# Optimization experiments

Hardware: AMD Instinct MI355X
Metric: run time of the kernel (lower is better)

The kernel has to match this reference:

```python
import jax, jax.numpy as jnp
import numpy as np

B, C, IMG, P = 8, 6, 384, 16
DIM, HEADS, DEPTH, MLP, NCLS = 768, 12, 4, 3072, 1000
N = (IMG // P) ** 2            # 576 patches
DH = DIM // HEADS              # 64
PATCH_DIM = C * P * P          # 1536


def setup_inputs() -> dict:
    key = jax.random.key(0)
    ks = jax.random.split(key, 13)
    f = lambda k, shp, s=0.02: jax.random.normal(k, shp, jnp.float32) * s
    return {
        "x": jax.random.normal(ks[0], (B, C, IMG, IMG), jnp.float32),
        "patch_w": f(ks[1], (PATCH_DIM, DIM)),
        "patch_b": f(ks[2], (DIM,)),
        "ln1_g": jnp.ones((DEPTH, DIM), jnp.float32),
        "ln1_b": jnp.zeros((DEPTH, DIM), jnp.float32),
        "w_qkv": f(ks[3], (DEPTH, DIM, 3 * DIM)),
        "bias_att": f(ks[4], (DEPTH, HEADS, N, N), 0.5),
        "w_out": f(ks[5], (DEPTH, DIM, DIM)),
        "ln2_g": jnp.ones((DEPTH, DIM), jnp.float32),
        "ln2_b": jnp.zeros((DEPTH, DIM), jnp.float32),
        "w1": f(ks[6], (DEPTH, DIM, MLP)),
        "b1": f(ks[7], (DEPTH, MLP)),
        "w2": f(ks[8], (DEPTH, MLP, DIM)),
        "b2": f(ks[9], (DEPTH, DIM)),
        "lnh_g": jnp.ones((DIM,), jnp.float32),
        "lnh_b": jnp.zeros((DIM,), jnp.float32),
        "w_head": f(ks[10], (DIM, NCLS)),
        "b_head": f(ks[11], (NCLS,)),
    }


def _ln(x, g, b, eps=1e-5):
    m = x.mean(-1, keepdims=True)
    v = ((x - m) ** 2).mean(-1, keepdims=True)
    return (x - m) * jax.lax.rsqrt(v + eps) * g + b


def _patchify(x, patch_w, patch_b):
    # Rearrange 'b c (h p1) (w p2) -> b (h w) (p1 p2 c)' then Linear(patch_dim, dim)
    b = x.shape[0]
    g = IMG // P
    x = x.reshape(b, C, g, P, g, P).transpose(0, 2, 4, 3, 5, 1).reshape(b, g * g, PATCH_DIM)
    return x @ patch_w + patch_b


def _forward(x, patch_w, patch_b, ln1_g, ln1_b, w_qkv, bias_att, w_out,
             ln2_g, ln2_b, w1, b1, w2, b2, lnh_g, lnh_b, w_head, b_head):
    scale = DH ** -0.5
    tok = _patchify(x, patch_w, patch_b)  # [B, N, DIM]; pos_info='mul_att_normed' -> no pos_embed added

    def block(t, p):
        l1g, l1b, wqkv, bias, wout, l2g, l2b, ww1, bb1, ww2, bb2 = p
        h = _ln(t, l1g, l1b)
        qkv = h @ wqkv                                     # [B, N, 3*DIM]
        q, k, v = jnp.split(qkv, 3, axis=-1)
        rs = lambda a: a.reshape(t.shape[0], N, HEADS, DH).transpose(0, 2, 1, 3)
        q, k, v = rs(q), rs(k), rs(v)                      # [B, H, N, DH]
        dots = jnp.einsum('bhid,bhjd->bhij', q, k) * scale
        # mul_att_normed: softmax(qk) * softmax(bias), renormalized over keys
        attn = jax.nn.softmax(dots, axis=-1) * jax.nn.softmax(bias, axis=-1)[None]
        attn = attn / attn.sum(-1, keepdims=True)
        o = jnp.einsum('bhij,bhjd->bhid', attn, v)
        o = o.transpose(0, 2, 1, 3).reshape(t.shape[0], N, DIM) @ wout
        t = t + o
        h2 = _ln(t, l2g, l2b)
        t = t + (jax.nn.gelu(h2 @ ww1 + bb1, approximate=False) @ ww2 + bb2)
        return t, None

    tok, _ = jax.lax.scan(block, tok,
                          (ln1_g, ln1_b, w_qkv, bias_att, w_out,
                           ln2_g, ln2_b, w1, b1, w2, b2))
    pooled = tok.mean(axis=1)                              # mean-pool tokens
    return _ln(pooled, lnh_g, lnh_b) @ w_head + b_head     # [B, NCLS]


def reference(x, patch_w, patch_b, ln1_g, ln1_b, w_qkv, bias_att, w_out,
              ln2_g, ln2_b, w1, b1, w2, b2, lnh_g, lnh_b, w_head, b_head):
    return _forward(x, patch_w, patch_b, ln1_g, ln1_b, w_qkv, bias_att, w_out,
                    ln2_g, ln2_b, w1, b1, w2, b2, lnh_g, lnh_b, w_head, b_head)
```

## Files before the change

kernel.cpp:

```cpp
#include <hip/hip_runtime.h>
#include <hip/hip_bf16.h>

typedef __attribute__((ext_vector_type(8))) short bf16x8;
typedef __attribute__((ext_vector_type(4))) float f32x4;

#define DEVI __device__ __forceinline__

DEVI unsigned short f2bf_bits(float f) {
    __hip_bfloat16 h = __float2bfloat16(f);
    return *reinterpret_cast<unsigned short*>(&h);
}
DEVI float bfbits2f(unsigned short u) {
    __hip_bfloat16 h = *reinterpret_cast<__hip_bfloat16*>(&u);
    return __bfloat162float(h);
}

DEVI void gload_lds16(const void* g, void* lds) {
    __builtin_amdgcn_global_load_lds(
        (const __attribute__((address_space(1))) unsigned int*)g,
        (__attribute__((address_space(3))) unsigned int*)lds, 16, 0, 0);
}

template <int N> DEVI void wait_vm() {
    if constexpr (N == 0) asm volatile("s_waitcnt vmcnt(0)" ::: "memory");
    else if constexpr (N == 3) asm volatile("s_waitcnt vmcnt(3)" ::: "memory");
    else if constexpr (N == 6) asm volatile("s_waitcnt vmcnt(6)" ::: "memory");
    else if constexpr (N == 12) asm volatile("s_waitcnt vmcnt(12)" ::: "memory");
    __builtin_amdgcn_sched_barrier(0);
}

DEVI int2 remap_cm(int bid, int total, int nrow) {
    int q = total >> 3, r = total & 7, x = bid & 7, l = bid >> 3;
    int seq = (x < r ? x * (q + 1) : r * (q + 1) + (x - r) * q) + l;
    return {seq % nrow, seq / nrow};
}

__global__ __launch_bounds__(256) void patchify_kernel(const float* __restrict__ x,
                                                       unsigned short* __restrict__ patches)
{
    size_t t8 = (size_t)blockIdx.x * 256 + threadIdx.x;
    int jq = (int)(t8 % 48);
    size_t t = t8 / 48;
    int r = (int)(t % 384); t /= 384;
    int c = (int)(t % 6);
    int b = (int)(t / 6);
    int j = jq * 8;
    int gh = r >> 4, p1 = r & 15, gw = j >> 4, p2 = j & 15;
    int prow = b * 576 + gh * 24 + gw;
    int pcol = c * 256 + p1 * 16 + p2;
    const float* src = x + ((((size_t)b * 6 + c) * 384 + r) * 384 + j);
    float4 v0 = ((const float4*)src)[0];
    float4 v1 = ((const float4*)src)[1];
    ushort u[8] = { f2bf_bits(v0.x), f2bf_bits(v0.y), f2bf_bits(v0.z), f2bf_bits(v0.w),
                    f2bf_bits(v1.x), f2bf_bits(v1.y), f2bf_bits(v1.z), f2bf_bits(v1.w) };
    *(int4*)&patches[(size_t)prow * 1536 + pcol] = *(int4*)u;
}

__global__ __launch_bounds__(256) void convT_patch_kernel(const float* __restrict__ W,
                                                          __hip_bfloat16* __restrict__ Wt)
{
    __shared__ float tile[32][33];
    int n0 = blockIdx.x * 32, kp0 = blockIdx.y * 32;
    int tx = threadIdx.x & 31, ty = threadIdx.x >> 5;
#pragma unroll
    for (int i = 0; i < 4; i++) {
        int kp = kp0 + ty + 8 * i;
        int k = (kp & 255) * 6 + (kp >> 8);
        tile[ty + 8 * i][tx] = W[(size_t)k * 768 + n0 + tx];
    }
    __syncthreads();
#pragma unroll
    for (int i = 0; i < 4; i++)
        Wt[(size_t)(n0 + ty + 8 * i) * 1536 + kp0 + tx] = __float2bfloat16(tile[tx][ty + 8 * i]);
}

DEVI void convT_body(const float* __restrict__ W, __hip_bfloat16* __restrict__ Wt,
                     int K, int N, int k0, int n0, int tid)
{
    __shared__ float tile[32][33];
    int tx = tid & 31, ty = tid >> 5;
#pragma unroll
    for (int i = 0; i < 4; i++)
        tile[ty + 8 * i][tx] = W[(size_t)(k0 + ty + 8 * i) * N + n0 + tx];
    __syncthreads();
#pragma unroll
    for (int i = 0; i < 4; i++)
        Wt[(size_t)(n0 + ty + 8 * i) * K + k0 + tx] = __float2bfloat16(tile[tx][ty + 8 * i]);
}

__global__ __launch_bounds__(256) void convT4_kernel(const float* __restrict__ wqkv,
                                                     const float* __restrict__ wout,
                                                     const float* __restrict__ w1,
                                                     const float* __restrict__ w2,
                                                     __hip_bfloat16* __restrict__ dst)
{
    int bt = blockIdx.x;
    const float* W; __hip_bfloat16* Wt; int K, N, lt;
    if (bt < 1728)      { W = wqkv; K = 768;  N = 2304; lt = bt;        Wt = dst; }
    else if (bt < 2304) { W = wout; K = 768;  N = 768;  lt = bt - 1728; Wt = dst + 1769472; }
    else if (bt < 4608) { W = w1;   K = 768;  N = 3072; lt = bt - 2304; Wt = dst + 2359296; }
    else                { W = w2;   K = 3072; N = 768;  lt = bt - 4608; Wt = dst + 4718592; }
    int tn = N >> 5;
    convT_body(W, Wt, K, N, (lt / tn) * 32, (lt % tn) * 32, threadIdx.x);
}

DEVI float ld_ln(const float* p) { return *p; }
DEVI float ld_ln(const __hip_bfloat16* p) { return __bfloat162float(*p); }
DEVI void st_ln(float* p, float v) { *p = v; }
DEVI void st_ln(__hip_bfloat16* p, float v) { *p = __float2bfloat16(v); }

template <typename InT, typename OutT>
__global__ __launch_bounds__(256) void ln_kernel(const InT* __restrict__ x,
                                                 const float* __restrict__ g,
                                                 const float* __restrict__ b,
                                                 OutT* __restrict__ out)
{
    int row = blockIdx.x, tid = threadIdx.x;
    const InT* xr = x + (size_t)row * 768;
    float v0 = ld_ln(&xr[tid]), v1 = ld_ln(&xr[tid + 256]), v2 = ld_ln(&xr[tid + 512]);
    float s = v0 + v1 + v2;
    float s2 = v0 * v0 + v1 * v1 + v2 * v2;
#pragma unroll
    for (int m = 32; m >= 1; m >>= 1) { s += __shfl_xor(s, m); s2 += __shfl_xor(s2, m); }
    __shared__ float red[8];
    int w = tid >> 6;
    if ((tid & 63) == 0) { red[w] = s; red[4 + w] = s2; }
    __syncthreads();
    s = red[0] + red[1] + red[2] + red[3];
    s2 = red[4] + red[5] + red[6] + red[7];
    float mean = s * (1.0f / 768.0f);
    float var = s2 * (1.0f / 768.0f) - mean * mean;
    float rstd = rsqrtf(var + 1e-5f);
    OutT* orow = out + (size_t)row * 768;
    st_ln(&orow[tid], (v0 - mean) * rstd * g[tid] + b[tid]);
    st_ln(&orow[tid + 256], (v1 - mean) * rstd * g[tid + 256] + b[tid + 256]);
    st_ln(&orow[tid + 512], (v2 - mean) * rstd * g[tid + 512] + b[tid + 512]);
}

template <bool BIAS, bool RESID>
__global__ __launch_bounds__(256, 3) void gemm_bt_kernel(
    const __hip_bfloat16* __restrict__ A,
    const __hip_bfloat16* __restrict__ Bt,
    const float* __restrict__ bias,
    const __hip_bfloat16* __restrict__ resid,
    __hip_bfloat16* __restrict__ Cb,
    int M, int N, int K, int nrow)
{
    constexpr int BM = 64, SL = 3;
    __shared__ __align__(16) __hip_bfloat16 As[3][BM * 32];
    __shared__ __align__(16) __hip_bfloat16 Bs[3][128 * 32];
    const int tid = threadIdx.x;
    const int wid = tid >> 6, lane = tid & 63;
    const int g = lane >> 4, l16 = lane & 15;
    const int wm = (wid >> 1) * 32, wn = (wid & 1) * 64;

    int2 bc = remap_cm(blockIdx.x, gridDim.x, nrow);
    const int bm = bc.x * BM, bn = bc.y * 128;

    const int sr = tid >> 2;
    const int csrc = (lane & 3) ^ ((lane >> 3) & 3);
    const int sdst = sr * 32 + (lane & 3) * 8;
    size_t aOff = (size_t)(bm + sr) * K + csrc * 8;
    size_t bOff[2];
#pragma unroll
    for (int i = 0; i < 2; i++) bOff[i] = (size_t)(bn + i * 64 + sr) * K + csrc * 8;

    auto stage = [&](__hip_bfloat16* asb, __hip_bfloat16* bsb, int tq) {
        const __hip_bfloat16* ap = A + tq * 32;
        const __hip_bfloat16* bp = Bt + tq * 32;
        gload_lds16(ap + aOff, asb + sdst);
#pragma unroll
        for (int i = 0; i < 2; i++) gload_lds16(bp + bOff[i], bsb + i * 2048 + sdst);
    };

    const int pSw = (l16 >> 1) & 3;
    f32x4 acc[2][4] = {};
    const int nt = K >> 5;

    stage(As[0], Bs[0], 0);
    stage(As[1], Bs[1], 1);
    stage(As[2], Bs[2], 2);
    wait_vm<2 * SL>();
    __builtin_amdgcn_s_barrier();
    __builtin_amdgcn_sched_barrier(0);

    for (int t = 0; t < nt; t += 3) {
#pragma unroll
        for (int u = 0; u < 3; u++) {
            const int tc = t + u;
            bf16x8 af[2], bfr[4];
#pragma unroll
            for (int mi = 0; mi < 2; mi++)
                af[mi] = *(const bf16x8*)&As[u][(wm + mi * 16 + l16) * 32 + ((g ^ pSw) << 3)];
#pragma unroll
            for (int ni = 0; ni < 4; ni++)
                bfr[ni] = *(const bf16x8*)&Bs[u][(wn + ni * 16 + l16) * 32 + ((g ^ pSw) << 3)];
#pragma unroll
            for (int mi = 0; mi < 2; mi++)
#pragma unroll
                for (int ni = 0; ni < 4; ni++)
                    acc[mi][ni] = __builtin_amdgcn_mfma_f32_16x16x32_bf16(af[mi], bfr[ni], acc[mi][ni], 0, 0, 0);

            asm volatile("s_waitcnt lgkmcnt(0)" ::: "memory");
            __builtin_amdgcn_sched_barrier(0);
            __builtin_amdgcn_s_barrier();
            __builtin_amdgcn_sched_barrier(0);

            if (tc + 3 < nt) stage(As[u], Bs[u], tc + 3);
            if (tc + 1 < nt) {
                if (tc + 4 <= nt)      wait_vm<2 * SL>();
                else if (tc + 3 == nt) wait_vm<SL>();
                else                   wait_vm<0>();
                __builtin_amdgcn_s_barrier();
                __builtin_amdgcn_sched_barrier(0);
            }
        }
    }

    __hip_bfloat16* scr = &As[0][0] + wid * (16 * 72);
#pragma unroll
    for (int mi = 0; mi < 2; mi++) {
#pragma unroll
        for (int ni = 0; ni < 4; ni++) {
            float bval = 0.0f;
            if (BIAS) bval = bias[bn + wn + ni * 16 + l16];
#pragma unroll
            for (int r = 0; r < 4; r++)
                scr[(4 * g + r) * 72 + ni * 16 + l16] = __float2bfloat16(acc[mi][ni][r] + bval);
        }
        asm volatile("s_waitcnt lgkmcnt(0)" ::: "memory");
        __builtin_amdgcn_sched_barrier(0);
#pragma unroll
        for (int q2 = 0; q2 < 2; q2++) {
            int row16 = q2 * 8 + (lane >> 3), ch = lane & 7;
            bf16x8 vv = *(const bf16x8*)&scr[row16 * 72 + ch * 8];
            int grow = bm + wm + mi * 16 + row16;
            size_t off = (size_t)grow * N + bn + wn + ch * 8;
            if (RESID) {
                bf16x8 rv = *(const bf16x8*)&resid[off];
#pragma unroll
                for (int e = 0; e < 8; e++)
                    vv[e] = (short)f2bf_bits(bfbits2f((unsigned short)vv[e]) + bfbits2f((unsigned short)rv[e]));
            }
            *(int4*)&Cb[off] = *(int4*)&vv;
        }
        asm volatile("s_waitcnt lgkmcnt(0)" ::: "memory");
        __builtin_amdgcn_sched_barrier(0);
    }
}

template <bool BIAS, bool GELU>
__global__ __launch_bounds__(256, 2) void gemm_wide_kernel(
    const __hip_bfloat16* __restrict__ A,
    const __hip_bfloat16* __restrict__ Bt,
    const float* __restrict__ bias,
    __hip_bfloat16* __restrict__ Cb,
    int M, int N, int K, int nrow)
{
    constexpr int SL = 6;
    __shared__ __align__(16) __hip_bfloat16 As[3][128 * 32];
    __shared__ __align__(16) __hip_bfloat16 Bs[3][256 * 32];
    const int tid = threadIdx.x;
    const int wid = tid >> 6, lane = tid & 63;
    const int g = lane >> 4, l16 = lane & 15;
    const int wm = (wid >> 1) * 64, wn = (wid & 1) * 128;

    int2 bc = remap_cm(blockIdx.x, gridDim.x, nrow);
    const int bm = bc.x * 128, bn = bc.y * 256;

    const int sr = tid >> 2;
    const int csrc = (lane & 3) ^ ((lane >> 3) & 3);
    const int sdst = sr * 32 + (lane & 3) * 8;
    size_t aOff[2], bOff[4];
#pragma unroll
    for (int i = 0; i < 2; i++) aOff[i] = (size_t)(bm + i * 64 + sr) * K + csrc * 8;
#pragma unroll
    for (int i = 0; i < 4; i++) bOff[i] = (size_t)(bn + i * 64 + sr) * K + csrc * 8;

    auto stage = [&](__hip_bfloat16* asb, __hip_bfloat16* bsb, int tq) {
        const __hip_bfloat16* ap = A + tq * 32;
        const __hip_bfloat16* bp = Bt + tq * 32;
#pragma unroll
        for (int i = 0; i < 2; i++) gload_lds16(ap + aOff[i], asb + i * 2048 + sdst);
#pragma unroll
        for (int i = 0; i < 4; i++) gload_lds16(bp + bOff[i], bsb + i * 2048 + sdst);
    };

    const int pSw = (l16 >> 1) & 3;
    f32x4 acc[4][8] = {};
    const int nt = K >> 5;

    stage(As[0], Bs[0], 0);
    stage(As[1], Bs[1], 1);
    stage(As[2], Bs[2], 2);
    wait_vm<2 * SL>();
    __builtin_amdgcn_s_barrier();
    __builtin_amdgcn_sched_barrier(0);

    for (int t = 0; t < nt; t += 3) {
#pragma unroll
        for (int u = 0; u < 3; u++) {
            const int tc = t + u;
            bf16x8 af[4], bfr[8];
#pragma unroll
            for (int mi = 0; mi < 4; mi++)
                af[mi] = *(const bf16x8*)&As[u][(wm + mi * 16 + l16) * 32 + ((g ^ pSw) << 3)];
#pragma unroll
            for (int ni = 0; ni < 8; ni++)
                bfr[ni] = *(const bf16x8*)&Bs[u][(wn + ni * 16 + l16) * 32 + ((g ^ pSw) << 3)];
#pragma unroll
            for (int mi = 0; mi < 4; mi++)
#pragma unroll
                for (int ni = 0; ni < 8; ni++)
                    acc[mi][ni] = __builtin_amdgcn_mfma_f32_16x16x32_bf16(af[mi], bfr[ni], acc[mi][ni], 0, 0, 0);

            asm volatile("s_waitcnt lgkmcnt(0)" ::: "memory");
            __builtin_amdgcn_sched_barrier(0);
            __builtin_amdgcn_s_barrier();
            __builtin_amdgcn_sched_barrier(0);

            if (tc + 3 < nt) stage(As[u], Bs[u], tc + 3);
            if (tc + 1 < nt) {
                if (tc + 4 <= nt)      wait_vm<2 * SL>();
                else if (tc + 3 == nt) wait_vm<SL>();
                else                   wait_vm<0>();
                __builtin_amdgcn_s_barrier();
                __builtin_amdgcn_sched_barrier(0);
            }
        }
    }

    __hip_bfloat16* scr = &As[0][0] + wid * (16 * 136);
#pragma unroll
    for (int mi = 0; mi < 4; mi++) {
#pragma unroll
        for (int ni = 0; ni < 8; ni++) {
            float bval = 0.0f;
            if (BIAS) bval = bias[bn + wn + ni * 16 + l16];
#pragma unroll
            for (int r = 0; r < 4; r++) {
                float v = acc[mi][ni][r] + bval;
                if (GELU) v = 0.5f * v * (1.0f + erff(v * 0.70710678118654752f));
                scr[(4 * g + r) * 136 + ni * 16 + l16] = __float2bfloat16(v);
            }
        }
        asm volatile("s_waitcnt lgkmcnt(0)" ::: "memory");
        __builtin_amdgcn_sched_barrier(0);
#pragma unroll
        for (int q2 = 0; q2 < 4; q2++) {
            int idx = q2 * 64 + lane;
            int row16 = idx >> 4, ch = idx & 15;
            bf16x8 vv = *(const bf16x8*)&scr[row16 * 136 + ch * 8];
            int grow = bm + wm + mi * 16 + row16;
            *(int4*)&Cb[(size_t)grow * N + bn + wn + ch * 8] = *(int4*)&vv;
        }
        asm volatile("s_waitcnt lgkmcnt(0)" ::: "memory");
        __builtin_amdgcn_sched_barrier(0);
    }
}

__global__ __launch_bounds__(256) void attn_kernel(const __hip_bfloat16* __restrict__ qkvb,
                                                   const float* __restrict__ bias,
                                                   unsigned short* __restrict__ o)
{
    const int seq = (blockIdx.x & 7) * 108 + (blockIdx.x >> 3);
    const int bb = seq & 7, qt = (seq >> 3) % 9, h = seq / 72;
    const int q0 = qt * 64;
    const int tid = threadIdx.x;
    const int wq = tid >> 6, lane = tid & 63, g = lane >> 4, l16 = lane & 15;

    __shared__ __align__(16) unsigned short Qs[64 * 72];
    __shared__ __align__(16) unsigned short Ks[64 * 72];
    __shared__ __align__(16) unsigned short Vt[64 * 72];
    __shared__ __align__(16) unsigned short Ps[4][16 * 72];

    {
        int r = tid >> 2, cb = (tid & 3) * 16;
        const int4* s4 = (const int4*)&qkvb[(size_t)(bb * 576 + q0 + r) * 2304 + h * 64 + cb];
        int4* d4 = (int4*)&Qs[r * 72 + cb];
        d4[0] = s4[0]; d4[1] = s4[1];
    }
    __syncthreads();
    bf16x8 qf0 = *(const bf16x8*)&Qs[(wq * 16 + l16) * 72 + g * 8];
    bf16x8 qf1 = *(const bf16x8*)&Qs[(wq * 16 + l16) * 72 + 32 + g * 8];

    float m_r[4] = {-1e30f, -1e30f, -1e30f, -1e30f};
    float l_r[4] = {0.f, 0.f, 0.f, 0.f};
    f32x4 oa[4] = {};
    const float* bias_h = bias + (size_t)h * 576 * 576;
    const float scale = 0.125f;

    for (int kt = 0; kt < 576; kt += 64) {
        {
            int r = tid >> 2, cb = (tid & 3) * 16;
            const int4* s4 = (const int4*)&qkvb[(size_t)(bb * 576 + kt + r) * 2304 + 768 + h * 64 + cb];
            int4* d4 = (int4*)&Ks[r * 72 + cb];
            d4[0] = s4[0]; d4[1] = s4[1];
            int key = tid & 63, d0 = (tid >> 6) * 16;
            const unsigned short* vs = (const unsigned short*)&qkvb[(size_t)(bb * 576 + kt + key) * 2304 + 1536 + h * 64 + d0];
            bf16x8 v0 = *(const bf16x8*)vs;
            bf16x8 v1 = *(const bf16x8*)(vs + 8);
#pragma unroll
            for (int e = 0; e < 8; e++) {
                Vt[(d0 + e) * 72 + key] = (unsigned short)v0[e];
                Vt[(d0 + 8 + e) * 72 + key] = (unsigned short)v1[e];
            }
        }
        __syncthreads();

        float bl[4][4];
#pragma unroll
        for (int kc = 0; kc < 4; kc++)
#pragma unroll
            for (int r = 0; r < 4; r++) {
                int q = q0 + wq * 16 + 4 * g + r;
                bl[kc][r] = bias_h[(size_t)q * 576 + kt + kc * 16 + l16];
            }

        f32x4 sc[4] = {};
        __builtin_amdgcn_s_setprio(1);
#pragma unroll
        for (int kc = 0; kc < 4; kc++) {
            bf16x8 kf0 = *(const bf16x8*)&Ks[(kc * 16 + l16) * 72 + g * 8];
            bf16x8 kf1 = *(const bf16x8*)&Ks[(kc * 16 + l16) * 72 + 32 + g * 8];
            sc[kc] = __builtin_amdgcn_mfma_f32_16x16x32_bf16(qf0, kf0, sc[kc], 0, 0, 0);
            sc[kc] = __builtin_amdgcn_mfma_f32_16x16x32_bf16(qf1, kf1, sc[kc], 0, 0, 0);
        }
        __builtin_amdgcn_s_setprio(0);

        float sv[4][4], mt[4] = {-1e30f, -1e30f, -1e30f, -1e30f};
#pragma unroll
        for (int kc = 0; kc < 4; kc++)
#pragma unroll
            for (int r = 0; r < 4; r++) {
                float s = sc[kc][r] * scale + bl[kc][r];
                sv[kc][r] = s;
                mt[r] = fmaxf(mt[r], s);
            }
#pragma unroll
        for (int r = 0; r < 4; r++)
#pragma unroll
            for (int m = 1; m < 16; m <<= 1) mt[r] = fmaxf(mt[r], __shfl_xor(mt[r], m));

        float sf[4];
#pragma unroll
        for (int r = 0; r < 4; r++) {
            float mn = fmaxf(m_r[r], mt[r]);
            sf[r] = __expf(m_r[r] - mn);
            m_r[r] = mn;
        }
        float rs[4] = {0.f, 0.f, 0.f, 0.f};
#pragma unroll
        for (int kc = 0; kc < 4; kc++)
#pragma unroll
            for (int r = 0; r < 4; r++) {
                float p = __expf(sv[kc][r] - m_r[r]);
                rs[r] += p;
                Ps[wq][(4 * g + r) * 72 + kc * 16 + l16] = f2bf_bits(p);
            }
#pragma unroll
        for (int r = 0; r < 4; r++) {
#pragma unroll
            for (int m = 1; m < 16; m <<= 1) rs[r] += __shfl_xor(rs[r], m);
            l_r[r] = l_r[r] * sf[r] + rs[r];
        }
#pragma unroll
        for (int dt = 0; dt < 4; dt++)
#pragma unroll
            for (int r = 0; r < 4; r++) oa[dt][r] *= sf[r];

        asm volatile("s_waitcnt lgkmcnt(0)" ::: "memory");

        __builtin_amdgcn_s_setprio(1);
#pragma unroll
        for (int s = 0; s < 2; s++) {
            bf16x8 pf = *(const bf16x8*)&Ps[wq][l16 * 72 + s * 32 + g * 8];
#pragma unroll
            for (int dt = 0; dt < 4; dt++) {
                bf16x8 vf = *(const bf16x8*)&Vt[(dt * 16 + l16) * 72 + s * 32 + g * 8];
                oa[dt] = __builtin_amdgcn_mfma_f32_16x16x32_bf16(pf, vf, oa[dt], 0, 0, 0);
            }
        }
        __builtin_amdgcn_s_setprio(0);
        __syncthreads();
    }

#pragma unroll
    for (int dt = 0; dt < 4; dt++)
#pragma unroll
        for (int r = 0; r < 4; r++) {
            int q = q0 + wq * 16 + 4 * g + r;
            float v = oa[dt][r] / l_r[r];
            o[(size_t)(bb * 576 + q) * 768 + h * 64 + dt * 16 + l16] = f2bf_bits(v);
        }
}

__global__ __launch_bounds__(256) void pool_kernel(const __hip_bfloat16* __restrict__ tok,
                                                   float* __restrict__ pooled)
{
    int d = blockIdx.x * 256 + threadIdx.x;
    int b = blockIdx.y;
    float s = 0.0f;
    for (int n = 0; n < 576; n++) s += __bfloat162float(tok[(size_t)(b * 576 + n) * 768 + d]);
    pooled[b * 768 + d] = s * (1.0f / 576.0f);
}

__global__ __launch_bounds__(256) void head_kernel(const float* __restrict__ lnp,
                                                   const float* __restrict__ w,
                                                   const float* __restrict__ bh,
                                                   float* __restrict__ out)
{
    int c = blockIdx.x * 256 + threadIdx.x;
    int b = blockIdx.y;
    if (c >= 1000) return;
    float s = bh[c];
    for (int d = 0; d < 768; d++) s += lnp[b * 768 + d] * w[(size_t)d * 1000 + c];
    out[b * 1000 + c] = s;
}

extern "C" void kernel_launch(void* const* d_in, const int* in_sizes, int n_in,
                              void* d_out, int out_size, void* d_ws, size_t ws_size,
                              hipStream_t stream)
{
    const float* x = (const float*)d_in[0];
    const float* patch_w = (const float*)d_in[1];
    const float* patch_b = (const float*)d_in[2];
    const float* ln1_g = (const float*)d_in[3];
    const float* ln1_b = (const float*)d_in[4];
    const float* w_qkv = (const float*)d_in[5];
    const float* bias_att = (const float*)d_in[6];
    const float* w_out = (const float*)d_in[7];
    const float* ln2_g = (const float*)d_in[8];
    const float* ln2_b = (const float*)d_in[9];
    const float* w1 = (const float*)d_in[10];
    const float* b1 = (const float*)d_in[11];
    const float* w2 = (const float*)d_in[12];
    const float* b2 = (const float*)d_in[13];
    const float* lnh_g = (const float*)d_in[14];
    const float* lnh_b = (const float*)d_in[15];
    const float* w_head = (const float*)d_in[16];
    const float* b_head = (const float*)d_in[17];
    float* out = (float*)d_out;

    char* ws = (char*)d_ws;
    __hip_bfloat16* tok = (__hip_bfloat16*)(ws + 0);
    __hip_bfloat16* qkv_bf = (__hip_bfloat16*)(ws + 14155776);
    float* pooled = (float*)(ws + 56623104);
    float* pooledln = (float*)(ws + 56647680);
    __hip_bfloat16* patches = (__hip_bfloat16*)(ws + 56672256);
    __hip_bfloat16* lw = patches;
    __hip_bfloat16* h_bf = (__hip_bfloat16*)(ws + 70828032);
    __hip_bfloat16* o_bf = (__hip_bfloat16*)(ws + 77905920);
    __hip_bfloat16* hid_bf = (__hip_bfloat16*)(ws + 84983808);
    __hip_bfloat16* wbuf = (__hip_bfloat16*)(ws + 113295360);

    patchify_kernel<<<3456, 256, 0, stream>>>(x, (unsigned short*)patches);
    convT_patch_kernel<<<dim3(24, 48), 256, 0, stream>>>(patch_w, wbuf);
    gemm_bt_kernel<true, false><<<432, 256, 0, stream>>>(
        patches, wbuf, patch_b, nullptr, tok, 4608, 768, 1536, 72);

    for (int l = 0; l < 4; l++) {
        convT4_kernel<<<6912, 256, 0, stream>>>(
            w_qkv + (size_t)l * 768 * 2304, w_out + (size_t)l * 768 * 768,
            w1 + (size_t)l * 768 * 3072, w2 + (size_t)l * 3072 * 768, lw);
        ln_kernel<__hip_bfloat16, __hip_bfloat16><<<4608, 256, 0, stream>>>(
            tok, ln1_g + l * 768, ln1_b + l * 768, h_bf);
        gemm_wide_kernel<false, false><<<324, 256, 0, stream>>>(
            h_bf, lw, nullptr, qkv_bf, 4608, 2304, 768, 36);
        attn_kernel<<<864, 256, 0, stream>>>(
            qkv_bf, bias_att + (size_t)l * 12 * 576 * 576, (unsigned short*)o_bf);
        gemm_bt_kernel<false, true><<<432, 256, 0, stream>>>(
            o_bf, lw + 1769472, nullptr, tok, tok, 4608, 768, 768, 72);
        ln_kernel<__hip_bfloat16, __hip_bfloat16><<<4608, 256, 0, stream>>>(
            tok, ln2_g + l * 768, ln2_b + l * 768, h_bf);
        gemm_wide_kernel<true, true><<<432, 256, 0, stream>>>(
            h_bf, lw + 2359296, b1 + l * 3072, hid_bf, 4608, 3072, 768, 36);
        gemm_bt_kernel<true, true><<<432, 256, 0, stream>>>(
            hid_bf, lw + 4718592, b2 + l * 768, tok, tok, 4608, 768, 3072, 72);
    }

    pool_kernel<<<dim3(3, 8), 256, 0, stream>>>(tok, pooled);
    ln_kernel<float, float><<<8, 256, 0, stream>>>(pooled, lnh_g, lnh_b, pooledln);
    head_kernel<<<dim3(4, 8), 256, 0, stream>>>(pooledln, w_head, b_head, out);
}
```

Measured before the change: 922.2 us.

## Widen gemm_bt K-tile to 64 and use grouped 2D block remapping

The narrow GEMM now stages 64-wide K slices per pipeline buffer instead of 32, with a new 8-way XOR swizzle and two MFMA sub-steps per stage. This halves the number of barriers and wait points per K. The LDS footprint doubles, so occupancy drops from 3 to 2 blocks per CU. Block-to-tile mapping changes to 4-row groups across columns for all GEMMs, aiming for better L2 reuse of A rows and B columns.

```diff
diff --git a/kernel.cpp b/kernel.cpp
--- a/kernel.cpp
+++ b/kernel.cpp
@@ -23,16 +23,17 @@
 
 template <int N> DEVI void wait_vm() {
     if constexpr (N == 0) asm volatile("s_waitcnt vmcnt(0)" ::: "memory");
-    else if constexpr (N == 3) asm volatile("s_waitcnt vmcnt(3)" ::: "memory");
     else if constexpr (N == 6) asm volatile("s_waitcnt vmcnt(6)" ::: "memory");
     else if constexpr (N == 12) asm volatile("s_waitcnt vmcnt(12)" ::: "memory");
     __builtin_amdgcn_sched_barrier(0);
 }
 
-DEVI int2 remap_cm(int bid, int total, int nrow) {
+DEVI int2 remap2d(int bid, int total, int gx) {
     int q = total >> 3, r = total & 7, x = bid & 7, l = bid >> 3;
     int seq = (x < r ? x * (q + 1) : r * (q + 1) + (x - r) * q) + l;
-    return {seq % nrow, seq / nrow};
+    int g4 = seq / (4 * gx);
+    int rem = seq - g4 * 4 * gx;
+    return {g4 * 4 + (rem & 3), rem >> 2};
 }
 
 __global__ __launch_bounds__(256) void patchify_kernel(const float* __restrict__ x,
@@ -138,44 +139,45 @@
 }
 
 template <bool BIAS, bool RESID>
-__global__ __launch_bounds__(256, 3) void gemm_bt_kernel(
+__global__ __launch_bounds__(256, 2) void gemm_bt_kernel(
     const __hip_bfloat16* __restrict__ A,
     const __hip_bfloat16* __restrict__ Bt,
     const float* __restrict__ bias,
     const __hip_bfloat16* __restrict__ resid,
     __hip_bfloat16* __restrict__ Cb,
-    int M, int N, int K, int nrow)
-{
-    constexpr int BM = 64, SL = 3;
-    __shared__ __align__(16) __hip_bfloat16 As[3][BM * 32];
-    __shared__ __align__(16) __hip_bfloat16 Bs[3][128 * 32];
+    int M, int N, int K, int gx)
+{
+    constexpr int BM = 64, SL = 6;
+    __shared__ __align__(16) __hip_bfloat16 As[3][BM * 64];
+    __shared__ __align__(16) __hip_bfloat16 Bs[3][128 * 64];
     const int tid = threadIdx.x;
     const int wid = tid >> 6, lane = tid & 63;
     const int g = lane >> 4, l16 = lane & 15;
     const int wm = (wid >> 1) * 32, wn = (wid & 1) * 64;
 
-    int2 bc = remap_cm(blockIdx.x, gridDim.x, nrow);
+    int2 bc = remap2d(blockIdx.x, gridDim.x, gx);
     const int bm = bc.x * BM, bn = bc.y * 128;
 
-    const int sr = tid >> 2;
-    const int csrc = (lane & 3) ^ ((lane >> 3) & 3);
-    const int sdst = sr * 32 + (lane & 3) * 8;
-    size_t aOff = (size_t)(bm + sr) * K + csrc * 8;
-    size_t bOff[2];
-#pragma unroll
-    for (int i = 0; i < 2; i++) bOff[i] = (size_t)(bn + i * 64 + sr) * K + csrc * 8;
+    const int sr32 = tid >> 3, ci = tid & 7;
+    const int cg = ci ^ (sr32 & 7);
+    const int sdst = tid * 8;
+    size_t aOff[2], bOff[4];
+#pragma unroll
+    for (int i = 0; i < 2; i++) aOff[i] = (size_t)(bm + i * 32 + sr32) * K + cg * 8;
+#pragma unroll
+    for (int i = 0; i < 4; i++) bOff[i] = (size_t)(bn + i * 32 + sr32) * K + cg * 8;
 
     auto stage = [&](__hip_bfloat16* asb, __hip_bfloat16* bsb, int tq) {
-        const __hip_bfloat16* ap = A + tq * 32;
-        const __hip_bfloat16* bp = Bt + tq * 32;
-        gload_lds16(ap + aOff, asb + sdst);
-#pragma unroll
-        for (int i = 0; i < 2; i++) gload_lds16(bp + bOff[i], bsb + i * 2048 + sdst);
+        const __hip_bfloat16* ap = A + tq * 64;
+        const __hip_bfloat16* bp = Bt + tq * 64;
+#pragma unroll
+        for (int i = 0; i < 2; i++) gload_lds16(ap + aOff[i], asb + i * 2048 + sdst);
+#pragma unroll
+        for (int i = 0; i < 4; i++) gload_lds16(bp + bOff[i], bsb + i * 2048 + sdst);
     };
 
-    const int pSw = (l16 >> 1) & 3;
     f32x4 acc[2][4] = {};
-    const int nt = K >> 5;
+    const int nt = K >> 6;
 
     stage(As[0], Bs[0], 0);
     stage(As[1], Bs[1], 1);
@@ -188,18 +190,24 @@
 #pragma unroll
         for (int u = 0; u < 3; u++) {
             const int tc = t + u;
-            bf16x8 af[2], bfr[4];
-#pragma unroll
-            for (int mi = 0; mi < 2; mi++)
-                af[mi] = *(const bf16x8*)&As[u][(wm + mi * 16 + l16) * 32 + ((g ^ pSw) << 3)];
-#pragma unroll
-            for (int ni = 0; ni < 4; ni++)
-                bfr[ni] = *(const bf16x8*)&Bs[u][(wn + ni * 16 + l16) * 32 + ((g ^ pSw) << 3)];
-#pragma unroll
-            for (int mi = 0; mi < 2; mi++)
+            bf16x8 af[2][2], bfr[2][4];
+#pragma unroll
+            for (int s = 0; s < 2; s++) {
+                const int cp = ((s * 4 + g) ^ (l16 & 7)) << 3;
+#pragma unroll
+                for (int mi = 0; mi < 2; mi++)
+                    af[s][mi] = *(const bf16x8*)&As[u][(wm + mi * 16 + l16) * 64 + cp];
 #pragma unroll
                 for (int ni = 0; ni < 4; ni++)
-                    acc[mi][ni] = __builtin_amdgcn_mfma_f32_16x16x32_bf16(af[mi], bfr[ni], acc[mi][ni], 0, 0, 0);
+                    bfr[s][ni] = *(const bf16x8*)&Bs[u][(wn + ni * 16 + l16) * 64 + cp];
+            }
+#pragma unroll
+            for (int s = 0; s < 2; s++)
+#pragma unroll
+                for (int mi = 0; mi < 2; mi++)
+#pragma unroll
+                    for (int ni = 0; ni < 4; ni++)
+                        acc[mi][ni] = __builtin_amdgcn_mfma_f32_16x16x32_bf16(af[s][mi], bfr[s][ni], acc[mi][ni], 0, 0, 0);
 
             asm volatile("s_waitcnt lgkmcnt(0)" ::: "memory");
             __builtin_amdgcn_sched_barrier(0);
@@ -255,7 +263,7 @@
     const __hip_bfloat16* __restrict__ Bt,
     const float* __restrict__ bias,
     __hip_bfloat16* __restrict__ Cb,
-    int M, int N, int K, int nrow)
+    int M, int N, int K, int gx)
 {
     constexpr int SL = 6;
     __shared__ __align__(16) __hip_bfloat16 As[3][128 * 32];
@@ -265,7 +273,7 @@
     const int g = lane >> 4, l16 = lane & 15;
     const int wm = (wid >> 1) * 64, wn = (wid & 1) * 128;
 
-    int2 bc = remap_cm(blockIdx.x, gridDim.x, nrow);
+    int2 bc = remap2d(blockIdx.x, gridDim.x, gx);
     const int bm = bc.x * 128, bn = bc.y * 256;
 
     const int sr = tid >> 2;
@@ -557,7 +565,7 @@
     patchify_kernel<<<3456, 256, 0, stream>>>(x, (unsigned short*)patches);
     convT_patch_kernel<<<dim3(24, 48), 256, 0, stream>>>(patch_w, wbuf);
     gemm_bt_kernel<true, false><<<432, 256, 0, stream>>>(
-        patches, wbuf, patch_b, nullptr, tok, 4608, 768, 1536, 72);
+        patches, wbuf, patch_b, nullptr, tok, 4608, 768, 1536, 6);
 
     for (int l = 0; l < 4; l++) {
         convT4_kernel<<<6912, 256, 0, stream>>>(
@@ -566,17 +574,17 @@
         ln_kernel<__hip_bfloat16, __hip_bfloat16><<<4608, 256, 0, stream>>>(
             tok, ln1_g + l * 768, ln1_b + l * 768, h_bf);
         gemm_wide_kernel<false, false><<<324, 256, 0, stream>>>(
-            h_bf, lw, nullptr, qkv_bf, 4608, 2304, 768, 36);
+            h_bf, lw, nullptr, qkv_bf, 4608, 2304, 768, 9);
         attn_kernel<<<864, 256, 0, stream>>>(
             qkv_bf, bias_att + (size_t)l * 12 * 576 * 576, (unsigned short*)o_bf);
         gemm_bt_kernel<false, true><<<432, 256, 0, stream>>>(
-            o_bf, lw + 1769472, nullptr, tok, tok, 4608, 768, 768, 72);
+            o_bf, lw + 1769472, nullptr, tok, tok, 4608, 768, 768, 6);
         ln_kernel<__hip_bfloat16, __hip_bfloat16><<<4608, 256, 0, stream>>>(
             tok, ln2_g + l * 768, ln2_b + l * 768, h_bf);
         gemm_wide_kernel<true, true><<<432, 256, 0, stream>>>(
-            h_bf, lw + 2359296, b1 + l * 3072, hid_bf, 4608, 3072, 768, 36);
+            h_bf, lw + 2359296, b1 + l * 3072, hid_bf, 4608, 3072, 768, 12);
         gemm_bt_kernel<true, true><<<432, 256, 0, stream>>>(
-            hid_bf, lw + 4718592, b2 + l * 768, tok, tok, 4608, 768, 3072, 72);
+            hid_bf, lw + 4718592, b2 + l * 768, tok, tok, 4608, 768, 3072, 6);
     }
 
     pool_kernel<<<dim3(3, 8), 256, 0, stream>>>(tok, pooled);
```

Result: faster. 845.4 us (-8.3%).
